# Kernel optimization log

Hardware: AMD Instinct MI355X
Metric: run time of the kernel (lower is better)

The kernel has to match this reference:

```python
import jax, jax.numpy as jnp
import numpy as np


def _sage(x_src, x_dst, src, dst, Wl, bl, Wr, n_dst):
    # gather source features along edges, mean-aggregate into destinations
    m = x_src[src]                                              # [E, H]
    s = jax.ops.segment_sum(m, dst, num_segments=n_dst)        # [N_dst, H]
    cnt = jax.ops.segment_sum(jnp.ones(src.shape, x_src.dtype), dst, num_segments=n_dst)
    mean = s / jnp.maximum(cnt, 1.0)[:, None]
    # SAGEConv: lin_l(agg) + lin_r(x_dst)  (lin_r has no bias in PyG)
    return mean @ Wl + bl + x_dst @ Wr


def setup_inputs() -> dict:
    key = jax.random.key(0)
    ks = jax.random.split(key, 24)
    N_C, N_T, E = 100000, 5000, 2000000
    D_C, D_T, H, H2 = 1024, 1280, 64, 32
    s = 0.05  # weight scale to keep residual stack numerically tame
    inp = {
        "x_comp": jax.random.normal(ks[0], (N_C, D_C), jnp.float32),
        "x_tgt": jax.random.normal(ks[1], (N_T, D_T), jnp.float32),
        "src_ct": jax.random.randint(ks[2], (E,), 0, N_C, jnp.int32),
        "dst_ct": jax.random.randint(ks[3], (E,), 0, N_T, jnp.int32),
        "src_tc": jax.random.randint(ks[4], (E,), 0, N_T, jnp.int32),
        "dst_tc": jax.random.randint(ks[5], (E,), 0, N_C, jnp.int32),
        "Wc": jax.random.normal(ks[6], (D_C, H), jnp.float32) * s,
        "bc": jax.random.normal(ks[7], (H,), jnp.float32) * s,
        "Wt": jax.random.normal(ks[8], (D_T, H), jnp.float32) * s,
        "bt": jax.random.normal(ks[9], (H,), jnp.float32) * s,
        "Wl_ct": jax.random.normal(ks[10], (3, H, H), jnp.float32) * s,
        "bl_ct": jax.random.normal(ks[11], (3, H), jnp.float32) * s,
        "Wr_ct": jax.random.normal(ks[12], (3, H, H), jnp.float32) * s,
        "Wl_tc": jax.random.normal(ks[13], (3, H, H), jnp.float32) * s,
        "bl_tc": jax.random.normal(ks[14], (3, H), jnp.float32) * s,
        "Wr_tc": jax.random.normal(ks[15], (3, H, H), jnp.float32) * s,
        "Wo1": jax.random.normal(ks[16], (H, H2), jnp.float32) * s,
        "bo1": jax.random.normal(ks[17], (H2,), jnp.float32) * s,
        "Wo2": jax.random.normal(ks[18], (H2, 1), jnp.float32) * s,
        "bo2": jax.random.normal(ks[19], (1,), jnp.float32) * s,
    }
    return inp


def reference(x_comp, x_tgt, src_ct, dst_ct, src_tc, dst_tc,
              Wc, bc, Wt, bt,
              Wl_ct, bl_ct, Wr_ct, Wl_tc, bl_tc, Wr_tc,
              Wo1, bo1, Wo2, bo2):
    xc = jax.nn.relu(x_comp @ Wc + bc)   # [N_C, H]
    xt = jax.nn.relu(x_tgt @ Wt + bt)    # [N_T, H]
    n_layers = Wl_ct.shape[0]
    for l in range(n_layers):
        # compound -> target updates targets; target -> compound updates compounds
        new_t = _sage(xc, xt, src_ct, dst_ct, Wl_ct[l], bl_ct[l], Wr_ct[l], xt.shape[0])
        new_c = _sage(xt, xc, src_tc, dst_tc, Wl_tc[l], bl_tc[l], Wr_tc[l], xc.shape[0])
        xc = jax.nn.relu(new_c) + xc
        xt = jax.nn.relu(new_t) + xt
    # output head on compounds (dropout is identity in eval)
    h = jax.nn.relu(xc @ Wo1 + bo1)
    return h @ Wo2 + bo2
```

## Files before the change

### kernel.cpp

```cpp
#include <hip/hip_runtime.h>

typedef unsigned int uint32;
typedef __bf16 bf16x8 __attribute__((ext_vector_type(8)));
typedef __bf16 bf16x4 __attribute__((ext_vector_type(4)));
typedef float f32x4 __attribute__((ext_vector_type(4)));

constexpr int N_C = 100000, N_T = 5000, E_EDGES = 2000000;
constexpr int D_C = 1024, D_T = 1280, H = 64, H2 = 32, NL = 3;
constexpr int PJC = (N_C + 63) / 64;
constexpr int PJT = (N_T + 63) / 64;
constexpr int NBC64 = (N_C + 63) / 64;

constexpr int CCH = 200;
constexpr int CHE = E_EDGES / CCH;
constexpr int SH_T = 4,  FB_T = 16;
constexpr int SH_C = 8,  FB_C = 256;
constexpr int NB_T_B = (N_T + FB_T - 1) / FB_T;
constexpr int NB_C_B = (N_C + FB_C - 1) / FB_C;
constexpr int NB_TOT = NB_T_B + NB_C_B;
constexpr int PB_T = 17; constexpr uint32 PM_T = 0x1FFFFu;
constexpr int PB_C = 13; constexpr uint32 PM_C = 0x1FFFu;

__device__ inline unsigned short f2bf(float f) {
  uint32 u = __float_as_uint(f);
  u += 0x7fffu + ((u >> 16) & 1u);
  return (unsigned short)(u >> 16);
}

__global__ __launch_bounds__(256) void prep_kernel(
    const float* __restrict__ Wc, const float* __restrict__ Wt,
    const float* __restrict__ Wl, const float* __restrict__ Wr,
    __bf16* __restrict__ WfC, __bf16* __restrict__ WfT, __bf16* __restrict__ WsT,
    int* __restrict__ T)
{
  int t = blockIdx.x * 256 + threadIdx.x;
  const int Z = NB_TOT;
  const int A = D_C * 64;
  const int B = D_T * 64;
  const int S = 6 * 64 * 64;
  if (t < Z) { T[t] = 0; return; }
  t -= Z;
  if (t < A) {
    int j = t & 7, l = (t >> 3) & 63, frag = t >> 9;
    int k0 = (frag >> 2) * 32, fn = frag & 3;
    int lm = l & 15, lk = l >> 4;
    WfC[t] = (__bf16)Wc[(size_t)(k0 + lk * 8 + j) * 64 + fn * 16 + lm];
    return;
  }
  t -= A;
  if (t < B) {
    int j = t & 7, l = (t >> 3) & 63, frag = t >> 9;
    int k0 = (frag >> 2) * 32, fn = frag & 3;
    int lm = l & 15, lk = l >> 4;
    WfT[t] = (__bf16)Wt[(size_t)(k0 + lk * 8 + j) * 64 + fn * 16 + lm];
    return;
  }
  t -= B;
  if (t < S) {
    int i = t >> 12;
    int r = t & 4095; int n = r & 63, k = r >> 6;
    const float* src = (i < 3) ? (Wl + (size_t)i * 4096) : (Wr + (size_t)(i - 3) * 4096);
    WsT[(size_t)i * 4096 + (size_t)n * 64 + k] = (__bf16)src[(size_t)k * 64 + n];
  }
}

template<int K>
__device__ __forceinline__ void projLDS_body(
    const float* __restrict__ x, const __bf16* __restrict__ Wf,
    const float* __restrict__ b, float* __restrict__ y,
    unsigned short* __restrict__ yh, int n, int bidx)
{
  constexpr int NT = K / 128;
  constexpr int ST = 152;
  __shared__ __align__(16) __bf16 sA[64 * ST];

  int t = threadIdx.x;
  int w = t >> 6, l = t & 63;
  int lm = l & 15, lk = l >> 4;
  int bbase = bidx * 64;
  int rowbase = bbase + w * 16;

  f32x4 acc[4] = {{0,0,0,0},{0,0,0,0},{0,0,0,0},{0,0,0,0}};

  int srow = t >> 5;
  int sc4  = t & 31;

  for (int tile = 0; tile < NT; ++tile) {
    if (tile) __syncthreads();
    float4 g[8];
#pragma unroll
    for (int r = 0; r < 8; ++r) {
      int row = srow + r * 8;
      int gr = bbase + row; if (gr >= n) gr = n - 1;
      g[r] = *(const float4*)(x + (size_t)gr * K + tile * 128 + sc4 * 4);
    }
#pragma unroll
    for (int r = 0; r < 8; ++r) {
      int row = srow + r * 8;
      bf16x4 v;
      v[0] = (__bf16)g[r].x; v[1] = (__bf16)g[r].y;
      v[2] = (__bf16)g[r].z; v[3] = (__bf16)g[r].w;
      *(bf16x4*)(sA + (size_t)row * ST + sc4 * 4) = v;
    }
    __syncthreads();

#pragma unroll
    for (int kk = 0; kk < 4; ++kk) {
      bf16x8 a0 = *(const bf16x8*)(sA + (size_t)(w * 16 + lm) * ST + kk * 32 + lk * 8);
#pragma unroll
      for (int fn = 0; fn < 4; ++fn) {
        bf16x8 bv = *(const bf16x8*)(Wf + ((size_t)(tile * 4 + kk) * 4 + fn) * 512 + l * 8);
        acc[fn] = __builtin_amdgcn_mfma_f32_16x16x32_bf16(a0, bv, acc[fn], 0, 0, 0);
      }
    }
  }

#pragma unroll
  for (int fn = 0; fn < 4; ++fn) {
    int col = fn * 16 + lm;
    float bb = b[col];
#pragma unroll
    for (int reg = 0; reg < 4; ++reg) {
      int row = rowbase + lk * 4 + reg;
      if (row < n) {
        float o = fmaxf(acc[fn][reg] + bb, 0.f);
        y[(size_t)row * 64 + col] = o;
        yh[(size_t)row * 64 + col] = f2bf(o);
      }
    }
  }
}

__global__ __launch_bounds__(256) void proj_kernel(
    const float* __restrict__ x_comp, const __bf16* __restrict__ WfC,
    const float* __restrict__ bc, float* __restrict__ xc, unsigned short* __restrict__ xch,
    const float* __restrict__ x_tgt, const __bf16* __restrict__ WfT,
    const float* __restrict__ bt, float* __restrict__ xt, unsigned short* __restrict__ xth)
{
  if (blockIdx.x < PJC) projLDS_body<D_C>(x_comp, WfC, bc, xc, xch, N_C, blockIdx.x);
  else                  projLDS_body<D_T>(x_tgt, WfT, bt, xt, xth, N_T, blockIdx.x - PJC);
}

__global__ __launch_bounds__(256) void csr1_kernel(
    const int* __restrict__ dst_ct, const int* __restrict__ dst_tc,
    int* __restrict__ h1, int* __restrict__ T)
{
  __shared__ int hist[NB_C_B];
  int graph = (blockIdx.x >= CCH) ? 1 : 0;
  int chunk = graph ? (blockIdx.x - CCH) : blockIdx.x;
  const int* dst = graph ? dst_tc : dst_ct;
  int NB = graph ? NB_C_B : NB_T_B;
  int SH = graph ? SH_C : SH_T;
  for (int i = threadIdx.x; i < NB; i += 256) hist[i] = 0;
  __syncthreads();
  int e0 = chunk * CHE;
  for (int i = threadIdx.x; i < CHE; i += 256)
    atomicAdd(&hist[dst[e0 + i] >> SH], 1);
  __syncthreads();
  int* h1g = h1 + (graph ? (size_t)NB_T_B * CCH : 0);
  int* Tg  = T + (graph ? NB_T_B : 0);
  for (int i = threadIdx.x; i < NB; i += 256) {
    int v = hist[i];
    h1g[(size_t)i * CCH + chunk] = v;
    if (v) atomicAdd(&Tg[i], v);
  }
}

__global__ __launch_bounds__(256) void csr2_kernel(
    const int* __restrict__ h1, const int* __restrict__ T, int* __restrict__ b1)
{
  __shared__ int sh[256];
  __shared__ int loc2[512];
  int b = blockIdx.x;
  int graph = (b >= NB_T_B) ? 1 : 0;
  int nb = graph ? NB_C_B : NB_T_B;
  int base = graph ? NB_T_B : 0;
  int bl = b - base;
  int tid = threadIdx.x;
  int v0 = (2 * tid     < nb) ? T[base + 2 * tid]     : 0;
  int v1 = (2 * tid + 1 < nb) ? T[base + 2 * tid + 1] : 0;
  int t = v0 + v1;
  sh[tid] = t;
  __syncthreads();
  for (int off = 1; off < 256; off <<= 1) {
    int xv = (tid >= off) ? sh[tid - off] : 0;
    __syncthreads(); sh[tid] += xv; __syncthreads();
  }
  int excl = sh[tid] - t;
  loc2[2 * tid] = excl;
  loc2[2 * tid + 1] = excl + v0;
  __syncthreads();
  int B = loc2[bl];
  const int* row = h1 + (graph ? (size_t)NB_T_B * CCH : 0) + (size_t)bl * CCH;
  int hv = (tid < CCH) ? row[tid] : 0;
  sh[tid] = hv;
  __syncthreads();
  for (int off = 1; off < 256; off <<= 1) {
    int xv = (tid >= off) ? sh[tid - off] : 0;
    __syncthreads(); sh[tid] += xv; __syncthreads();
  }
  int e2 = sh[tid] - hv;
  if (tid < CCH) {
    int* b1g = b1 + (graph ? (size_t)NB_T_B * CCH : 0) + (size_t)bl * CCH;
    b1g[tid] = B + e2;
  }
}

__global__ __launch_bounds__(256) void csr3_kernel(
    const int* __restrict__ src_ct, const int* __restrict__ dst_ct,
    const int* __restrict__ src_tc, const int* __restrict__ dst_tc,
    const int* __restrict__ b1, uint32* __restrict__ packT_t, uint32* __restrict__ packT_c)
{
  __shared__ int cur[NB_C_B];
  int graph = (blockIdx.x >= CCH) ? 1 : 0;
  int chunk = graph ? (blockIdx.x - CCH) : blockIdx.x;
  const int* dst = graph ? dst_tc : dst_ct;
  const int* src = graph ? src_tc : src_ct;
  uint32* packT = graph ? packT_c : packT_t;
  int NB = graph ? NB_C_B : NB_T_B;
  int SH = graph ? SH_C : SH_T;
  int SB = graph ? PB_C : PB_T;
  const int* b1g = b1 + (graph ? (size_t)NB_T_B * CCH : 0);
  for (int i = threadIdx.x; i < NB; i += 256) cur[i] = b1g[(size_t)i * CCH + chunk];
  __syncthreads();
  int e0 = chunk * CHE;
  for (int i = threadIdx.x; i < CHE; i += 256) {
    int d = dst[e0 + i], s = src[e0 + i];
    int p = atomicAdd(&cur[d >> SH], 1);
    packT[p] = ((uint32)d << SB) | (uint32)s;
  }
}

__global__ __launch_bounds__(256) void csr4_kernel(
    const int* __restrict__ b1, const uint32* __restrict__ packT_t,
    const uint32* __restrict__ packT_c,
    int* __restrict__ rowptr_t, int* __restrict__ col_ct,
    int* __restrict__ rowptr_c, int* __restrict__ col_tc)
{
  __shared__ int hist[FB_C];
  __shared__ int exc[256];
  int b = blockIdx.x;
  int graph = (b >= NB_T_B) ? 1 : 0;
  int bl = graph ? (b - NB_T_B) : b;
  int nb = graph ? NB_C_B : NB_T_B;
  int FB = graph ? FB_C : FB_T;
  int SB = graph ? PB_C : PB_T;
  uint32 SM = graph ? PM_C : PM_T;
  uint32 FMM = (uint32)(FB - 1);
  int N  = graph ? N_C : N_T;
  const uint32* packT = graph ? packT_c : packT_t;
  int* rowptr = graph ? rowptr_c : rowptr_t;
  int* col    = graph ? col_tc : col_ct;
  const int* b1g = b1 + (graph ? (size_t)NB_T_B * CCH : 0);
  int seg0 = b1g[(size_t)bl * CCH];
  int seg1 = (bl + 1 < nb) ? b1g[(size_t)(bl + 1) * CCH] : E_EDGES;
  int tid = threadIdx.x;
  if (tid < FB) hist[tid] = 0;
  __syncthreads();
  for (int i = seg0 + tid; i < seg1; i += 256)
    atomicAdd(&hist[(packT[i] >> SB) & FMM], 1);
  __syncthreads();
  int hv = (tid < FB) ? hist[tid] : 0;
  exc[tid] = hv;
  __syncthreads();
  for (int off = 1; off < 256; off <<= 1) {
    int xv = (tid >= off) ? exc[tid - off] : 0;
    __syncthreads(); exc[tid] += xv; __syncthreads();
  }
  int excl = exc[tid] - hv;
  __syncthreads();
  if (tid < FB) {
    int gbin = bl * FB + tid;
    if (gbin <= N) rowptr[gbin] = seg0 + excl;
    hist[tid] = seg0 + excl;
  }
  __syncthreads();
  for (int i = seg0 + tid; i < seg1; i += 256) {
    uint32 pk = packT[i];
    int p = atomicAdd(&hist[(pk >> SB) & FMM], 1);
    col[p] = (int)(pk & SM);
  }
}

__global__ __launch_bounds__(256) void layerT_kernel(
    const unsigned short* __restrict__ xch_a, const float* __restrict__ xt_a,
    const int* __restrict__ rowptr_t, const int* __restrict__ col_ct,
    const float* __restrict__ Wl_t, const float* __restrict__ bl_t, const float* __restrict__ Wr_t,
    float* __restrict__ xt_n, unsigned short* __restrict__ xth_n)
{
  __shared__ __align__(16) float part[4][64];
  __shared__ __align__(16) float opart[4][64];

  int l = threadIdx.x & 63, w = threadIdx.x >> 6;
  int d = l & 31, half = l >> 5;

  int r = blockIdx.x;
  int start = rowptr_t[r], end = rowptr_t[r + 1];
  int deg = end - start;
  int quarter = (deg + 3) >> 2;
  int js = start + w * quarter;
  int je = js + quarter; if (je > end) je = end;
  const uint32* xp = (const uint32*)xch_a;
  float a0 = 0.f, a1 = 0.f;
  int j0 = js + half;
  for (int j = j0; j < je; j += 16) {
    int idx[8]; uint32 vv[8];
#pragma unroll
    for (int k = 0; k < 8; ++k) {
      int jj = j + 2 * k;
      idx[k] = col_ct[(jj < je) ? jj : j];
    }
#pragma unroll
    for (int k = 0; k < 8; ++k) vv[k] = xp[(size_t)idx[k] * 32 + d];
#pragma unroll
    for (int k = 0; k < 8; ++k) {
      bool m = (j + 2 * k) < je;
      a0 += m ? __uint_as_float(vv[k] << 16) : 0.f;
      a1 += m ? __uint_as_float(vv[k] & 0xffff0000u) : 0.f;
    }
  }
  a0 += __shfl_xor(a0, 32, 64);
  a1 += __shfl_xor(a1, 32, 64);
  if (half == 0) *(float2*)&part[w][2 * d] = make_float2(a0, a1);
  __syncthreads();
  float m = (part[0][l] + part[1][l] + part[2][l] + part[3][l])
            * ((deg > 0) ? (1.0f / (float)deg) : 0.f);
  float xv = xt_a[(size_t)r * 64 + l];
  float o = 0.f;
  int k0 = w * 16;
#pragma unroll
  for (int kk = 0; kk < 16; ++kk) {
    int k = k0 + kk;
    float mk = __uint_as_float(__builtin_amdgcn_readlane(__float_as_uint(m), k));
    float xk = __uint_as_float(__builtin_amdgcn_readlane(__float_as_uint(xv), k));
    o = fmaf(mk, Wl_t[k * 64 + l], o);
    o = fmaf(xk, Wr_t[k * 64 + l], o);
  }
  opart[w][l] = o;
  __syncthreads();
  if (w == 0) {
    float oo = opart[0][l] + opart[1][l] + opart[2][l] + opart[3][l] + bl_t[l];
    float res = fmaxf(oo, 0.f) + xv;
    xt_n[(size_t)r * 64 + l] = res;
    xth_n[(size_t)r * 64 + l] = f2bf(res);
  }
}

__global__ __launch_bounds__(256) void layerC_kernel(
    const unsigned short* __restrict__ xch_a,
    const unsigned short* __restrict__ xth_a, const int* __restrict__ rowptr_c,
    const int* __restrict__ col_tc,
    const __bf16* __restrict__ WlT, const __bf16* __restrict__ WrT,
    const float* __restrict__ bl_c, const float* __restrict__ xc_a,
    float* __restrict__ xc_n, unsigned short* __restrict__ xch_n)
{
  __shared__ __align__(16) uint32 smem_u[64 * 36];

  int l = threadIdx.x & 63, w = threadIdx.x >> 6;
  int d = l & 31, half = l >> 5;

  int bbase = blockIdx.x * 64;

  int rp_idx = bbase + w * 16 + ((l <= 16) ? l : 16);
  if (rp_idx > N_C) rp_idx = N_C;
  int rpl = rowptr_c[rp_idx];
  const uint32* xp = (const uint32*)xth_a;

#pragma unroll 1
  for (int t = 0; t < 8; ++t) {
    int s = __shfl(rpl, 2 * t + half, 64);
    int e = __shfl(rpl, 2 * t + half + 1, 64);
    float a0 = 0.f, a1 = 0.f;
    int n = e - s;
    for (int j = 0; j < n; j += 8) {
      int idx[8]; uint32 vv[8];
#pragma unroll
      for (int k = 0; k < 8; ++k) {
        int jj = s + j + k;
        idx[k] = col_tc[(jj < e) ? jj : s];
      }
#pragma unroll
      for (int k = 0; k < 8; ++k) vv[k] = xp[(size_t)idx[k] * 32 + d];
#pragma unroll
      for (int k = 0; k < 8; ++k) {
        bool m = (j + k) < n;
        a0 += m ? __uint_as_float(vv[k] << 16) : 0.f;
        a1 += m ? __uint_as_float(vv[k] & 0xffff0000u) : 0.f;
      }
    }
    float inv = (n > 0) ? (1.0f / (float)n) : 0.f;
    uint32 packed = (uint32)f2bf(a0 * inv) | ((uint32)f2bf(a1 * inv) << 16);
    smem_u[(size_t)(w * 16 + 2 * t + half) * 36 + d] = packed;
  }
  __syncthreads();

  int lm = l & 15, lk = l >> 4;
  int base = bbase + w * 16;
  int r0 = base + lm; if (r0 >= N_C) r0 = N_C - 1;
  const unsigned short* x0 = xch_a + (size_t)r0 * 64 + lk * 8;
  const __bf16* wl = WlT + (size_t)lm * 64 + lk * 8;
  const __bf16* wr = WrT + (size_t)lm * 64 + lk * 8;

  f32x4 acc[4] = {{0,0,0,0},{0,0,0,0},{0,0,0,0},{0,0,0,0}};

#pragma unroll
  for (int ks = 0; ks < 64; ks += 32) {
    bf16x8 am0 = *(const bf16x8*)&smem_u[(size_t)(w * 16 + lm) * 36 + lk * 4 + (ks >> 1)];
    bf16x8 ax0 = *(const bf16x8*)(x0 + ks);
#pragma unroll
    for (int fn = 0; fn < 4; ++fn) {
      bf16x8 bl_v = *(const bf16x8*)(wl + (size_t)fn * 16 * 64 + ks);
      bf16x8 br_v = *(const bf16x8*)(wr + (size_t)fn * 16 * 64 + ks);
      acc[fn] = __builtin_amdgcn_mfma_f32_16x16x32_bf16(am0, bl_v, acc[fn], 0, 0, 0);
      acc[fn] = __builtin_amdgcn_mfma_f32_16x16x32_bf16(ax0, br_v, acc[fn], 0, 0, 0);
    }
  }

#pragma unroll
  for (int fn = 0; fn < 4; ++fn) {
    int col = fn * 16 + lm;
    float bb = bl_c[col];
#pragma unroll
    for (int reg = 0; reg < 4; ++reg) {
      int row = base + lk * 4 + reg;
      if (row < N_C) {
        float xv = xc_a[(size_t)row * 64 + col];
        float o = fmaxf(acc[fn][reg] + bb, 0.f) + xv;
        xc_n[(size_t)row * 64 + col] = o;
        xch_n[(size_t)row * 64 + col] = f2bf(o);
      }
    }
  }
}

__global__ __launch_bounds__(256) void head_kernel(
    const float* __restrict__ xc, const float* __restrict__ Wo1,
    const float* __restrict__ bo1, const float* __restrict__ Wo2,
    const float* __restrict__ bo2, float* __restrict__ out, int n)
{
  int lane = threadIdx.x & 63;
  int wid = blockIdx.x * (blockDim.x >> 6) + (threadIdx.x >> 6);
  if (wid >= n) return;
  float xv = xc[(size_t)wid * 64 + lane];
  float h = (lane < H2) ? bo1[lane] : 0.f;
  const float* wcol = Wo1 + ((lane < H2) ? lane : 0);
#pragma unroll 8
  for (int k = 0; k < 64; ++k) {
    float xk = __uint_as_float(__builtin_amdgcn_readlane(__float_as_uint(xv), k));
    h = fmaf(xk, wcol[k * H2], h);
  }
  float v = (lane < H2) ? fmaxf(h, 0.f) * Wo2[lane] : 0.f;
#pragma unroll
  for (int off = 32; off > 0; off >>= 1) v += __shfl_down(v, off, 64);
  if (lane == 0) out[wid] = v + bo2[0];
}

extern "C" void kernel_launch(void* const* d_in, const int* in_sizes, int n_in,
                              void* d_out, int out_size, void* d_ws, size_t ws_size,
                              hipStream_t stream)
{
  const float* x_comp = (const float*)d_in[0];
  const float* x_tgt  = (const float*)d_in[1];
  const int*   src_ct = (const int*)d_in[2];
  const int*   dst_ct = (const int*)d_in[3];
  const int*   src_tc = (const int*)d_in[4];
  const int*   dst_tc = (const int*)d_in[5];
  const float* Wc    = (const float*)d_in[6];
  const float* bc    = (const float*)d_in[7];
  const float* Wt    = (const float*)d_in[8];
  const float* bt    = (const float*)d_in[9];
  const float* Wl_ct = (const float*)d_in[10];
  const float* bl_ct = (const float*)d_in[11];
  const float* Wr_ct = (const float*)d_in[12];
  const float* Wl_tc = (const float*)d_in[13];
  const float* bl_tc = (const float*)d_in[14];
  const float* Wr_tc = (const float*)d_in[15];
  const float* Wo1   = (const float*)d_in[16];
  const float* bo1   = (const float*)d_in[17];
  const float* Wo2   = (const float*)d_in[18];
  const float* bo2   = (const float*)d_in[19];
  float* out = (float*)d_out;

  char* p = (char*)d_ws;
  auto alloc = [&](size_t bytes) {
    char* q = p;
    p += (bytes + 255) & ~(size_t)255;
    return q;
  };
  float* xc   = (float*)alloc((size_t)N_C * H * 4);
  float* xt   = (float*)alloc((size_t)N_T * H * 4);
  float* xc_b = (float*)alloc((size_t)N_C * H * 4);
  float* xt_b = (float*)alloc((size_t)N_T * H * 4);
  unsigned short* xch   = (unsigned short*)alloc((size_t)N_C * H * 2);
  unsigned short* xth   = (unsigned short*)alloc((size_t)N_T * H * 2);
  unsigned short* xch_b = (unsigned short*)alloc((size_t)N_C * H * 2);
  unsigned short* xth_b = (unsigned short*)alloc((size_t)N_T * H * 2);
  __bf16* WfC = (__bf16*)alloc((size_t)D_C * H * 2);
  __bf16* WfT = (__bf16*)alloc((size_t)D_T * H * 2);
  __bf16* WsT = (__bf16*)alloc((size_t)6 * H * H * 2);
  int*    h1        = (int*)alloc((size_t)NB_TOT * CCH * 4);
  int*    b1        = (int*)alloc((size_t)NB_TOT * CCH * 4);
  int*    T         = (int*)alloc((size_t)NB_TOT * 4);
  uint32* packT_t   = (uint32*)alloc((size_t)E_EDGES * 4);
  uint32* packT_c   = (uint32*)alloc((size_t)E_EDGES * 4);
  int*    rowptr_t  = (int*)alloc((size_t)(N_T + 1) * 4);
  int*    rowptr_c  = (int*)alloc((size_t)(N_C + 1) * 4);
  int*    col_ct    = (int*)alloc((size_t)E_EDGES * 4);
  int*    col_tc    = (int*)alloc((size_t)E_EDGES * 4);

  const int PREP_TOTAL = NB_TOT + D_C * 64 + D_T * 64 + 6 * 4096;
  prep_kernel<<<dim3((PREP_TOTAL + 255) / 256), dim3(256), 0, stream>>>(
      Wc, Wt, Wl_tc, Wr_tc, WfC, WfT, WsT, T);

  proj_kernel<<<dim3(PJC + PJT), dim3(256), 0, stream>>>(
      x_comp, WfC, bc, xc, xch, x_tgt, WfT, bt, xt, xth);

  csr1_kernel<<<dim3(2 * CCH), dim3(256), 0, stream>>>(dst_ct, dst_tc, h1, T);
  csr2_kernel<<<dim3(NB_TOT), dim3(256), 0, stream>>>(h1, T, b1);
  csr3_kernel<<<dim3(2 * CCH), dim3(256), 0, stream>>>(
      src_ct, dst_ct, src_tc, dst_tc, b1, packT_t, packT_c);
  csr4_kernel<<<dim3(NB_TOT), dim3(256), 0, stream>>>(
      b1, packT_t, packT_c, rowptr_t, col_ct, rowptr_c, col_tc);

  float* xc_a = xc; float* xt_a = xt;
  float* xc_n = xc_b; float* xt_n = xt_b;
  unsigned short* xch_a = xch; unsigned short* xth_a = xth;
  unsigned short* xch_n = xch_b; unsigned short* xth_n = xth_b;
  for (int l = 0; l < NL; ++l) {
    layerT_kernel<<<dim3(N_T), dim3(256), 0, stream>>>(
        xch_a, xt_a, rowptr_t, col_ct,
        Wl_ct + (size_t)l * H * H, bl_ct + (size_t)l * H, Wr_ct + (size_t)l * H * H,
        xt_n, xth_n);
    layerC_kernel<<<dim3(NBC64), dim3(256), 0, stream>>>(
        xch_a, xth_a, rowptr_c, col_tc,
        WsT + (size_t)l * H * H, WsT + (size_t)(3 + l) * H * H,
        bl_tc + (size_t)l * H, xc_a, xc_n, xch_n);
    float* t;
    t = xc_a; xc_a = xc_n; xc_n = t;
    t = xt_a; xt_a = xt_n; xt_n = t;
    unsigned short* th;
    th = xch_a; xch_a = xch_n; xch_n = th;
    th = xth_a; xth_a = xth_n; xth_n = th;
  }

  head_kernel<<<dim3((N_C + 3) / 4), dim3(256), 0, stream>>>(xc_a, Wo1, bo1, Wo2, bo2, out, N_C);
}
```

Baseline: 598.4 us.

## Fuse target and compound layer kernels into one launch; widen CSR chunk count

Merges the per-layer target-update and compound-update kernels into a single launch, where the first N_T blocks do target rows and the rest do compound tiles, sharing one shared-memory buffer. Both updates read only the previous layer's state, so they can run concurrently and the tail of one no longer leaves the GPU partly idle before the other starts. It also raises the CSR-build chunk count from 200 to 800 and makes the prefix-scan kernel handle four chunks per thread. That gives the histogram and scatter passes more parallelism at the cost of a larger per-chunk offset table.

```diff
diff --git a/kernel.cpp b/kernel.cpp
--- a/kernel.cpp
+++ b/kernel.cpp
@@ -11,7 +11,7 @@
 constexpr int PJT = (N_T + 63) / 64;
 constexpr int NBC64 = (N_C + 63) / 64;
 
-constexpr int CCH = 200;
+constexpr int CCH = 800;
 constexpr int CHE = E_EDGES / CCH;
 constexpr int SH_T = 4,  FB_T = 16;
 constexpr int SH_C = 8,  FB_C = 256;
@@ -192,18 +192,25 @@
   __syncthreads();
   int B = loc2[bl];
   const int* row = h1 + (graph ? (size_t)NB_T_B * CCH : 0) + (size_t)bl * CCH;
-  int hv = (tid < CCH) ? row[tid] : 0;
-  sh[tid] = hv;
+  int c0 = tid * 4;
+  int h0 = (c0 + 0 < CCH) ? row[c0 + 0] : 0;
+  int h1v = (c0 + 1 < CCH) ? row[c0 + 1] : 0;
+  int h2 = (c0 + 2 < CCH) ? row[c0 + 2] : 0;
+  int h3 = (c0 + 3 < CCH) ? row[c0 + 3] : 0;
+  int ts = h0 + h1v + h2 + h3;
+  __syncthreads();
+  sh[tid] = ts;
   __syncthreads();
   for (int off = 1; off < 256; off <<= 1) {
     int xv = (tid >= off) ? sh[tid - off] : 0;
     __syncthreads(); sh[tid] += xv; __syncthreads();
   }
-  int e2 = sh[tid] - hv;
-  if (tid < CCH) {
-    int* b1g = b1 + (graph ? (size_t)NB_T_B * CCH : 0) + (size_t)bl * CCH;
-    b1g[tid] = B + e2;
-  }
+  int e2 = sh[tid] - ts;
+  int* b1g = b1 + (graph ? (size_t)NB_T_B * CCH : 0) + (size_t)bl * CCH;
+  if (c0 + 0 < CCH) b1g[c0 + 0] = B + e2;
+  if (c0 + 1 < CCH) b1g[c0 + 1] = B + e2 + h0;
+  if (c0 + 2 < CCH) b1g[c0 + 2] = B + e2 + h0 + h1v;
+  if (c0 + 3 < CCH) b1g[c0 + 3] = B + e2 + h0 + h1v + h2;
 }
 
 __global__ __launch_bounds__(256) void csr3_kernel(
@@ -282,72 +289,11 @@
   }
 }
 
-__global__ __launch_bounds__(256) void layerT_kernel(
+__global__ __launch_bounds__(256) void layer_kernel(
     const unsigned short* __restrict__ xch_a, const float* __restrict__ xt_a,
     const int* __restrict__ rowptr_t, const int* __restrict__ col_ct,
     const float* __restrict__ Wl_t, const float* __restrict__ bl_t, const float* __restrict__ Wr_t,
-    float* __restrict__ xt_n, unsigned short* __restrict__ xth_n)
-{
-  __shared__ __align__(16) float part[4][64];
-  __shared__ __align__(16) float opart[4][64];
-
-  int l = threadIdx.x & 63, w = threadIdx.x >> 6;
-  int d = l & 31, half = l >> 5;
-
-  int r = blockIdx.x;
-  int start = rowptr_t[r], end = rowptr_t[r + 1];
-  int deg = end - start;
-  int quarter = (deg + 3) >> 2;
-  int js = start + w * quarter;
-  int je = js + quarter; if (je > end) je = end;
-  const uint32* xp = (const uint32*)xch_a;
-  float a0 = 0.f, a1 = 0.f;
-  int j0 = js + half;
-  for (int j = j0; j < je; j += 16) {
-    int idx[8]; uint32 vv[8];
-#pragma unroll
-    for (int k = 0; k < 8; ++k) {
-      int jj = j + 2 * k;
-      idx[k] = col_ct[(jj < je) ? jj : j];
-    }
-#pragma unroll
-    for (int k = 0; k < 8; ++k) vv[k] = xp[(size_t)idx[k] * 32 + d];
-#pragma unroll
-    for (int k = 0; k < 8; ++k) {
-      bool m = (j + 2 * k) < je;
-      a0 += m ? __uint_as_float(vv[k] << 16) : 0.f;
-      a1 += m ? __uint_as_float(vv[k] & 0xffff0000u) : 0.f;
-    }
-  }
-  a0 += __shfl_xor(a0, 32, 64);
-  a1 += __shfl_xor(a1, 32, 64);
-  if (half == 0) *(float2*)&part[w][2 * d] = make_float2(a0, a1);
-  __syncthreads();
-  float m = (part[0][l] + part[1][l] + part[2][l] + part[3][l])
-            * ((deg > 0) ? (1.0f / (float)deg) : 0.f);
-  float xv = xt_a[(size_t)r * 64 + l];
-  float o = 0.f;
-  int k0 = w * 16;
-#pragma unroll
-  for (int kk = 0; kk < 16; ++kk) {
-    int k = k0 + kk;
-    float mk = __uint_as_float(__builtin_amdgcn_readlane(__float_as_uint(m), k));
-    float xk = __uint_as_float(__builtin_amdgcn_readlane(__float_as_uint(xv), k));
-    o = fmaf(mk, Wl_t[k * 64 + l], o);
-    o = fmaf(xk, Wr_t[k * 64 + l], o);
-  }
-  opart[w][l] = o;
-  __syncthreads();
-  if (w == 0) {
-    float oo = opart[0][l] + opart[1][l] + opart[2][l] + opart[3][l] + bl_t[l];
-    float res = fmaxf(oo, 0.f) + xv;
-    xt_n[(size_t)r * 64 + l] = res;
-    xth_n[(size_t)r * 64 + l] = f2bf(res);
-  }
-}
-
-__global__ __launch_bounds__(256) void layerC_kernel(
-    const unsigned short* __restrict__ xch_a,
+    float* __restrict__ xt_n, unsigned short* __restrict__ xth_n,
     const unsigned short* __restrict__ xth_a, const int* __restrict__ rowptr_c,
     const int* __restrict__ col_tc,
     const __bf16* __restrict__ WlT, const __bf16* __restrict__ WrT,
@@ -355,11 +301,67 @@
     float* __restrict__ xc_n, unsigned short* __restrict__ xch_n)
 {
   __shared__ __align__(16) uint32 smem_u[64 * 36];
+  float (*part)[64]  = (float(*)[64])smem_u;
+  float (*opart)[64] = (float(*)[64])(smem_u + 256);
 
   int l = threadIdx.x & 63, w = threadIdx.x >> 6;
   int d = l & 31, half = l >> 5;
 
-  int bbase = blockIdx.x * 64;
+  if (blockIdx.x < N_T) {
+    int r = blockIdx.x;
+    int start = rowptr_t[r], end = rowptr_t[r + 1];
+    int deg = end - start;
+    int quarter = (deg + 3) >> 2;
+    int js = start + w * quarter;
+    int je = js + quarter; if (je > end) je = end;
+    const uint32* xp = (const uint32*)xch_a;
+    float a0 = 0.f, a1 = 0.f;
+    int j0 = js + half;
+    for (int j = j0; j < je; j += 16) {
+      int idx[8]; uint32 vv[8];
+#pragma unroll
+      for (int k = 0; k < 8; ++k) {
+        int jj = j + 2 * k;
+        idx[k] = col_ct[(jj < je) ? jj : j];
+      }
+#pragma unroll
+      for (int k = 0; k < 8; ++k) vv[k] = xp[(size_t)idx[k] * 32 + d];
+#pragma unroll
+      for (int k = 0; k < 8; ++k) {
+        bool m = (j + 2 * k) < je;
+        a0 += m ? __uint_as_float(vv[k] << 16) : 0.f;
+        a1 += m ? __uint_as_float(vv[k] & 0xffff0000u) : 0.f;
+      }
+    }
+    a0 += __shfl_xor(a0, 32, 64);
+    a1 += __shfl_xor(a1, 32, 64);
+    if (half == 0) *(float2*)&part[w][2 * d] = make_float2(a0, a1);
+    __syncthreads();
+    float m = (part[0][l] + part[1][l] + part[2][l] + part[3][l])
+              * ((deg > 0) ? (1.0f / (float)deg) : 0.f);
+    float xv = xt_a[(size_t)r * 64 + l];
+    float o = 0.f;
+    int k0 = w * 16;
+#pragma unroll
+    for (int kk = 0; kk < 16; ++kk) {
+      int k = k0 + kk;
+      float mk = __uint_as_float(__builtin_amdgcn_readlane(__float_as_uint(m), k));
+      float xk = __uint_as_float(__builtin_amdgcn_readlane(__float_as_uint(xv), k));
+      o = fmaf(mk, Wl_t[k * 64 + l], o);
+      o = fmaf(xk, Wr_t[k * 64 + l], o);
+    }
+    opart[w][l] = o;
+    __syncthreads();
+    if (w == 0) {
+      float oo = opart[0][l] + opart[1][l] + opart[2][l] + opart[3][l] + bl_t[l];
+      float res = fmaxf(oo, 0.f) + xv;
+      xt_n[(size_t)r * 64 + l] = res;
+      xth_n[(size_t)r * 64 + l] = f2bf(res);
+    }
+    return;
+  }
+
+  int bbase = (blockIdx.x - N_T) * 64;
 
   int rp_idx = bbase + w * 16 + ((l <= 16) ? l : 16);
   if (rp_idx > N_C) rp_idx = N_C;
@@ -527,12 +529,11 @@
   unsigned short* xch_a = xch; unsigned short* xth_a = xth;
   unsigned short* xch_n = xch_b; unsigned short* xth_n = xth_b;
   for (int l = 0; l < NL; ++l) {
-    layerT_kernel<<<dim3(N_T), dim3(256), 0, stream>>>(
+    layer_kernel<<<dim3(N_T + NBC64), dim3(256), 0, stream>>>(
         xch_a, xt_a, rowptr_t, col_ct,
         Wl_ct + (size_t)l * H * H, bl_ct + (size_t)l * H, Wr_ct + (size_t)l * H * H,
-        xt_n, xth_n);
-    layerC_kernel<<<dim3(NBC64), dim3(256), 0, stream>>>(
-        xch_a, xth_a, rowptr_c, col_tc,
+        xt_n, xth_n,
+        xth_a, rowptr_c, col_tc,
         WsT + (size_t)l * H * H, WsT + (size_t)(3 + l) * H * H,
         bl_tc + (size_t)l * H, xc_a, xc_n, xch_n);
     float* t;
```

Measured after the change: 628.7 us. +5.1%, slower.
